# Kernel optimization log

Measured on AMD Instinct MI355X. Metric: run time of the kernel, lower is better.

## Reference

```python
import jax, jax.numpy as jnp
import numpy as np

N_NODES = 50000
N_EDGES = 100000
IN_FEATS = 63          # nodes has 64 cols: 63 features + 1 root flag
HIDDEN = 64
NUM_REL = 8
OUT_DIM = 1


def setup_inputs() -> dict:
    key = jax.random.key(0)
    k1, k2, k3, k4, k5, k6, k7 = jax.random.split(key, 7)
    nodes = jax.random.normal(k1, (N_NODES, IN_FEATS + 1), dtype=jnp.float32)
    senders = jax.random.randint(k2, (N_EDGES,), 0, N_NODES, dtype=jnp.int32)
    receivers = jax.random.randint(k3, (N_EDGES,), 0, N_NODES, dtype=jnp.int32)
    edge_types = jax.random.randint(k4, (N_EDGES,), 0, NUM_REL, dtype=jnp.int32)
    n_node = jnp.ones((1,), dtype=jnp.int32) * N_NODES
    # lecun_normal for kernels: std = 1/sqrt(fan_in)
    kernels = jax.random.normal(k5, (NUM_REL, IN_FEATS, HIDDEN), dtype=jnp.float32) / np.sqrt(IN_FEATS)
    dense_w = jax.random.normal(k6, (HIDDEN, OUT_DIM), dtype=jnp.float32) / np.sqrt(HIDDEN)
    dense_b = jnp.zeros((OUT_DIM,), dtype=jnp.float32)
    return {"nodes": nodes, "senders": senders, "receivers": receivers,
            "edge_types": edge_types, "n_node": n_node,
            "kernels": kernels, "dense_w": dense_w, "dense_b": dense_b}


def reference(nodes, senders, receivers, edge_types, n_node, kernels, dense_w, dense_b):
    num_nodes = nodes.shape[0]
    h = nodes[:, :-1]                     # [N, IN_FEATS]
    is_root = nodes[:, -1:]               # [N, 1]

    # --- single RGCN layer (hidden_dims=[64]) ---
    sender_feats = h[senders]             # [E, IN_FEATS] gather
    edge_kernels = kernels[edge_types]    # [E, IN_FEATS, HIDDEN] relation gather
    messages = jnp.einsum('eif,ei->ef', edge_kernels, sender_feats)  # [E, HIDDEN]

    ones = jnp.ones_like(senders, dtype=jnp.float32)
    sender_deg = jax.ops.segment_sum(ones, senders, num_segments=num_nodes)
    receiver_deg = jax.ops.segment_sum(ones, receivers, num_segments=num_nodes)
    norm_s = jax.lax.rsqrt(jnp.maximum(sender_deg, 1.0))
    norm_r = jax.lax.rsqrt(jnp.maximum(receiver_deg, 1.0))

    messages = messages * norm_s[senders, None]
    agg = jax.ops.segment_sum(messages, receivers, num_segments=num_nodes)
    agg = agg * norm_r[:, None]
    h = jax.nn.relu(agg)                  # [N, HIDDEN]

    # --- root pooling (num_graphs == 1) ---
    num_graphs = n_node.shape[0]
    segment_ids = jnp.repeat(jnp.arange(num_graphs), repeats=num_nodes // num_graphs)
    graph_emb = jax.ops.segment_sum(h * is_root, segment_ids, num_segments=num_graphs)  # [1, HIDDEN]

    out = graph_emb @ dense_w + dense_b   # [1, OUT_DIM]
    return jnp.squeeze(out, axis=0)
```

## Files before the change

### kernel.cpp

```cpp
#include <hip/hip_runtime.h>

#define NN 50000
#define NE 100000
#define IN_F 63
#define HID 64
#define NREL 8
#define CHUNK 64
#define R1_BLOCKS 2048

__global__ __launch_bounds__(256) void deg_kernel(const int* __restrict__ senders,
                                                  const int* __restrict__ receivers,
                                                  float* __restrict__ sdeg,
                                                  float* __restrict__ rdeg) {
    int e = blockIdx.x * 256 + threadIdx.x;
    if (e < NE) {
        atomicAdd(&sdeg[senders[e]], 1.0f);
        atomicAdd(&rdeg[receivers[e]], 1.0f);
    }
}

__global__ __launch_bounds__(256) void edge_kernel(const float* __restrict__ nodes,
                                                   const int* __restrict__ senders,
                                                   const int* __restrict__ receivers,
                                                   const int* __restrict__ etypes,
                                                   const float* __restrict__ kernels,
                                                   const float* __restrict__ sdeg,
                                                   float* __restrict__ agg) {
    const int lane = threadIdx.x & 63;
    const int t = blockIdx.x & (NREL - 1);
    const int chunk = (blockIdx.x >> 3) * 4 + (threadIdx.x >> 6);
    const int base = chunk * CHUNK;
    if (base >= NE) return;
    const int lim = min(base + CHUNK, NE);

    float kcol[IN_F];
    const float* Kt = kernels + (size_t)t * IN_F * HID;
#pragma unroll
    for (int i = 0; i < IN_F; ++i) kcol[i] = Kt[i * HID + lane];

    const int e = base + lane;
    int pack_l = 0, ty = -1, s_tmp = 0;
    if (e < lim) {
        ty     = etypes[e];
        s_tmp  = senders[e];
        pack_l = s_tmp | (receivers[e] << 16);
    }
    float ns_l = 1.0f;
    if (ty == t) ns_l = rsqrtf(fmaxf(sdeg[s_tmp], 1.0f));

    unsigned long long m = __ballot(ty == t);
    while (m) {
        const int i0 = __builtin_ctzll(m); m &= m - 1;
        const bool has2 = (m != 0);
        const int i1 = has2 ? __builtin_ctzll(m) : i0;
        if (has2) m &= m - 1;

        const int   p0  = __builtin_amdgcn_readfirstlane(__shfl(pack_l, i0));
        const float ns0 = __shfl(ns_l, i0);
        const int   p1  = __builtin_amdgcn_readfirstlane(__shfl(pack_l, i1));
        const float ns1 = __shfl(ns_l, i1);
        const int s0 = p0 & 0xFFFF, r0 = ((unsigned)p0) >> 16;
        const int s1 = p1 & 0xFFFF, r1 = ((unsigned)p1) >> 16;

        const float4* xa = (const float4*)(nodes + (size_t)s0 * (IN_F + 1));
        const float4* xb = (const float4*)(nodes + (size_t)s1 * (IN_F + 1));
        float a0 = 0.f, a1 = 0.f, a2 = 0.f, a3 = 0.f;
        float b0 = 0.f, b1 = 0.f, b2 = 0.f, b3 = 0.f;
#pragma unroll
        for (int j = 0; j < 16; ++j) {
            const float4 va = xa[j];
            const float4 vb = xb[j];
            a0 = fmaf(kcol[4 * j + 0], va.x, a0);
            a1 = fmaf(kcol[4 * j + 1], va.y, a1);
            a2 = fmaf(kcol[4 * j + 2], va.z, a2);
            if (4 * j + 3 < IN_F) a3 = fmaf(kcol[4 * j + 3], va.w, a3);
            b0 = fmaf(kcol[4 * j + 0], vb.x, b0);
            b1 = fmaf(kcol[4 * j + 1], vb.y, b1);
            b2 = fmaf(kcol[4 * j + 2], vb.z, b2);
            if (4 * j + 3 < IN_F) b3 = fmaf(kcol[4 * j + 3], vb.w, b3);
        }
        atomicAdd(&agg[(size_t)r0 * HID + lane], ((a0 + a1) + (a2 + a3)) * ns0);
        if (has2)
            atomicAdd(&agg[(size_t)r1 * HID + lane], ((b0 + b1) + (b2 + b3)) * ns1);
    }
}

__global__ __launch_bounds__(256) void readout1_kernel(const float* __restrict__ nodes,
                                                       const float* __restrict__ agg,
                                                       const float* __restrict__ rdeg,
                                                       const float* __restrict__ w,
                                                       float* __restrict__ partial) {
    __shared__ float wsum[4];
    const int lane = threadIdx.x & 63;
    const int wid  = threadIdx.x >> 6;
    const int gw = blockIdx.x * 4 + wid;
    const int nw = R1_BLOCKS * 4;
    const float wf = w[lane];

    float local = 0.f;
    for (int n = gw; n < NN; n += nw) {
        float a = agg[(size_t)n * HID + lane];
        float nr = rsqrtf(fmaxf(rdeg[n], 1.0f));
        float root = nodes[(size_t)n * (IN_F + 1) + IN_F];
        local += fmaxf(a * nr, 0.f) * root;
    }
    float v = local * wf;
#pragma unroll
    for (int o = 32; o > 0; o >>= 1) v += __shfl_xor(v, o, 64);
    if (lane == 0) wsum[wid] = v;
    __syncthreads();
    if (threadIdx.x == 0)
        partial[blockIdx.x] = (wsum[0] + wsum[1]) + (wsum[2] + wsum[3]);
}

__global__ __launch_bounds__(256) void readout2_kernel(const float* __restrict__ partial,
                                                       const float* __restrict__ b,
                                                       float* __restrict__ out) {
    __shared__ float wsum[4];
    const int lane = threadIdx.x & 63;
    const int wid  = threadIdx.x >> 6;
    float v = 0.f;
    for (int i = threadIdx.x; i < R1_BLOCKS; i += 256) v += partial[i];
#pragma unroll
    for (int o = 32; o > 0; o >>= 1) v += __shfl_xor(v, o, 64);
    if (lane == 0) wsum[wid] = v;
    __syncthreads();
    if (threadIdx.x == 0)
        out[0] = (wsum[0] + wsum[1]) + (wsum[2] + wsum[3]) + b[0];
}

extern "C" void kernel_launch(void* const* d_in, const int* in_sizes, int n_in,
                              void* d_out, int out_size, void* d_ws, size_t ws_size,
                              hipStream_t stream) {
    const float* nodes     = (const float*)d_in[0];
    const int*   senders   = (const int*)d_in[1];
    const int*   receivers = (const int*)d_in[2];
    const int*   etypes    = (const int*)d_in[3];
    const float* kernels   = (const float*)d_in[5];
    const float* dense_w   = (const float*)d_in[6];
    const float* dense_b   = (const float*)d_in[7];
    float* out = (float*)d_out;

    float* agg     = (float*)d_ws;
    float* sdeg    = agg + (size_t)NN * HID;
    float* rdeg    = sdeg + NN;
    float* partial = rdeg + NN;

    size_t zero_bytes = ((size_t)NN * HID + 2 * (size_t)NN) * sizeof(float);
    (void)hipMemsetAsync(d_ws, 0, zero_bytes, stream);

    deg_kernel<<<(NE + 255) / 256, 256, 0, stream>>>(senders, receivers, sdeg, rdeg);

    const int nchunks = (NE + CHUNK - 1) / CHUNK;
    const int cgroups = (nchunks + 3) / 4;
    const int blocks  = cgroups * NREL;
    edge_kernel<<<blocks, 256, 0, stream>>>(nodes, senders, receivers, etypes,
                                            kernels, sdeg, agg);

    readout1_kernel<<<R1_BLOCKS, 256, 0, stream>>>(nodes, agg, rdeg, dense_w, partial);
    readout2_kernel<<<1, 256, 0, stream>>>(partial, dense_b, out);
}
```

Before: 124.3 us.

## Bucket edges by relation type and compute messages per-lane with transposed kernels

Adds a counting-sort pass that groups edges by relation into padded per-type segments, with the sender norm precomputed. A transposed copy of the relation kernels lets each lane compute one edge's full 64-wide message from a register-held feature row with uniform weight loads. Messages are staged in rotated shared memory and scattered with coalesced atomics. This replaces the old scheme in which each relation block scanned every edge chunk and processed matching edges with wave-serial shuffles, at the cost of three extra small kernel launches and heavy register use per lane.

```diff
diff --git a/kernel.cpp b/kernel.cpp
--- a/kernel.cpp
+++ b/kernel.cpp
@@ -5,8 +5,9 @@
 #define IN_F 63
 #define HID 64
 #define NREL 8
-#define CHUNK 64
 #define R1_BLOCKS 2048
+#define EPAD (NE + NREL * 63)
+#define EBLKS ((EPAD + 63) / 64)
 
 __global__ __launch_bounds__(256) void deg_kernel(const int* __restrict__ senders,
                                                   const int* __restrict__ receivers,
@@ -19,69 +20,116 @@
     }
 }
 
-__global__ __launch_bounds__(256) void edge_kernel(const float* __restrict__ nodes,
-                                                   const int* __restrict__ senders,
-                                                   const int* __restrict__ receivers,
-                                                   const int* __restrict__ etypes,
-                                                   const float* __restrict__ kernels,
-                                                   const float* __restrict__ sdeg,
+__global__ __launch_bounds__(256) void ktrans_kernel(const float* __restrict__ K,
+                                                     float* __restrict__ KT) {
+    int idx = blockIdx.x * 256 + threadIdx.x;
+    if (idx < NREL * HID * IN_F) {
+        int t = idx / (HID * IN_F);
+        int rem = idx - t * (HID * IN_F);
+        int f = rem / IN_F;
+        int i = rem - f * IN_F;
+        KT[idx] = K[(size_t)t * IN_F * HID + i * HID + f];
+    }
+}
+
+__global__ __launch_bounds__(256) void rsort_kernel(const int* __restrict__ senders,
+                                                    const int* __restrict__ receivers,
+                                                    const int* __restrict__ etypes,
+                                                    const float* __restrict__ sdeg,
+                                                    int* __restrict__ gcur,
+                                                    int* __restrict__ sr32,
+                                                    float* __restrict__ ns_srt) {
+    __shared__ int lcnt[NREL], lloc[NREL];
+    if (threadIdx.x < NREL) lcnt[threadIdx.x] = 0;
+    __syncthreads();
+    const int e = blockIdx.x * 256 + threadIdx.x;
+    int t = 0, rank = 0, s = 0, r = 0;
+    if (e < NE) {
+        t = etypes[e]; s = senders[e]; r = receivers[e];
+        rank = atomicAdd(&lcnt[t], 1);
+    }
+    __syncthreads();
+    if (threadIdx.x < NREL)
+        lloc[threadIdx.x] = atomicAdd(&gcur[threadIdx.x], lcnt[threadIdx.x]);
+    __syncthreads();
+    if (e < NE) {
+        const int pos = t * NE + lloc[t] + rank;
+        sr32[pos] = s | (r << 16);
+        ns_srt[pos] = rsqrtf(fmaxf(sdeg[s], 1.0f));
+    }
+}
+
+__global__ __launch_bounds__(64) void padclear_kernel(const int* __restrict__ gcur,
+                                                      int* __restrict__ sr32,
+                                                      float* __restrict__ ns_srt) {
+    const int t = blockIdx.x;
+    const int c = gcur[t];
+    const int end = (c + 63) & ~63;
+    const int i = c + threadIdx.x;
+    if (i < end) {
+        sr32[t * NE + i] = 0;
+        ns_srt[t * NE + i] = 0.f;
+    }
+}
+
+__global__ __launch_bounds__(64) void edgeT_kernel(const float* __restrict__ nodes,
+                                                   const float* __restrict__ KT,
+                                                   const int* __restrict__ sr32,
+                                                   const float* __restrict__ ns_srt,
+                                                   const int* __restrict__ gcur,
                                                    float* __restrict__ agg) {
-    const int lane = threadIdx.x & 63;
-    const int t = blockIdx.x & (NREL - 1);
-    const int chunk = (blockIdx.x >> 3) * 4 + (threadIdx.x >> 6);
-    const int base = chunk * CHUNK;
-    if (base >= NE) return;
-    const int lim = min(base + CHUNK, NE);
-
-    float kcol[IN_F];
-    const float* Kt = kernels + (size_t)t * IN_F * HID;
-#pragma unroll
-    for (int i = 0; i < IN_F; ++i) kcol[i] = Kt[i * HID + lane];
-
-    const int e = base + lane;
-    int pack_l = 0, ty = -1, s_tmp = 0;
-    if (e < lim) {
-        ty     = etypes[e];
-        s_tmp  = senders[e];
-        pack_l = s_tmp | (receivers[e] << 16);
-    }
-    float ns_l = 1.0f;
-    if (ty == t) ns_l = rsqrtf(fmaxf(sdeg[s_tmp], 1.0f));
-
-    unsigned long long m = __ballot(ty == t);
-    while (m) {
-        const int i0 = __builtin_ctzll(m); m &= m - 1;
-        const bool has2 = (m != 0);
-        const int i1 = has2 ? __builtin_ctzll(m) : i0;
-        if (has2) m &= m - 1;
-
-        const int   p0  = __builtin_amdgcn_readfirstlane(__shfl(pack_l, i0));
-        const float ns0 = __shfl(ns_l, i0);
-        const int   p1  = __builtin_amdgcn_readfirstlane(__shfl(pack_l, i1));
-        const float ns1 = __shfl(ns_l, i1);
-        const int s0 = p0 & 0xFFFF, r0 = ((unsigned)p0) >> 16;
-        const int s1 = p1 & 0xFFFF, r1 = ((unsigned)p1) >> 16;
-
-        const float4* xa = (const float4*)(nodes + (size_t)s0 * (IN_F + 1));
-        const float4* xb = (const float4*)(nodes + (size_t)s1 * (IN_F + 1));
+    __shared__ float outb[64 * HID];
+    const int lane = threadIdx.x;
+
+    int base = 0, t = -1, local = 0;
+#pragma unroll
+    for (int tt = 0; tt < NREL; ++tt) {
+        const int seg = (gcur[tt] + 63) & ~63;
+        if (t < 0 && blockIdx.x * 64 < base + seg) { t = tt; local = blockIdx.x * 64 - base; }
+        base += seg;
+    }
+    if (t < 0) return;
+
+    const int e = t * NE + local + lane;
+    const int sr = sr32[e];
+    const float nsv = ns_srt[e];
+    const int s = sr & 0xFFFF;
+
+    float x[HID];
+    const float4* x4 = (const float4*)(nodes + (size_t)s * HID);
+#pragma unroll
+    for (int j = 0; j < 16; ++j) {
+        const float4 v = x4[j];
+        x[4 * j + 0] = v.x; x[4 * j + 1] = v.y;
+        x[4 * j + 2] = v.z; x[4 * j + 3] = v.w;
+    }
+
+    const float* KTt = KT + (size_t)t * HID * IN_F;
+#pragma unroll 2
+    for (int f = 0; f < HID; ++f) {
+        const float* kf = KTt + f * IN_F;
         float a0 = 0.f, a1 = 0.f, a2 = 0.f, a3 = 0.f;
-        float b0 = 0.f, b1 = 0.f, b2 = 0.f, b3 = 0.f;
-#pragma unroll
-        for (int j = 0; j < 16; ++j) {
-            const float4 va = xa[j];
-            const float4 vb = xb[j];
-            a0 = fmaf(kcol[4 * j + 0], va.x, a0);
-            a1 = fmaf(kcol[4 * j + 1], va.y, a1);
-            a2 = fmaf(kcol[4 * j + 2], va.z, a2);
-            if (4 * j + 3 < IN_F) a3 = fmaf(kcol[4 * j + 3], va.w, a3);
-            b0 = fmaf(kcol[4 * j + 0], vb.x, b0);
-            b1 = fmaf(kcol[4 * j + 1], vb.y, b1);
-            b2 = fmaf(kcol[4 * j + 2], vb.z, b2);
-            if (4 * j + 3 < IN_F) b3 = fmaf(kcol[4 * j + 3], vb.w, b3);
+#pragma unroll
+        for (int i = 0; i < 60; i += 4) {
+            a0 = fmaf(kf[i + 0], x[i + 0], a0);
+            a1 = fmaf(kf[i + 1], x[i + 1], a1);
+            a2 = fmaf(kf[i + 2], x[i + 2], a2);
+            a3 = fmaf(kf[i + 3], x[i + 3], a3);
         }
-        atomicAdd(&agg[(size_t)r0 * HID + lane], ((a0 + a1) + (a2 + a3)) * ns0);
-        if (has2)
-            atomicAdd(&agg[(size_t)r1 * HID + lane], ((b0 + b1) + (b2 + b3)) * ns1);
+        a0 = fmaf(kf[60], x[60], a0);
+        a1 = fmaf(kf[61], x[61], a1);
+        a2 = fmaf(kf[62], x[62], a2);
+        outb[lane * HID + ((f + lane) & 63)] = (a0 + a1) + (a2 + a3);
+    }
+    __syncthreads();
+
+    const int r_l = ((unsigned)sr) >> 16;
+    for (int e2 = 0; e2 < 64; ++e2) {
+        const float nsu = __shfl(nsv, e2);
+        if (nsu == 0.f) continue;
+        const int rr = __shfl(r_l, e2);
+        const float val = outb[e2 * HID + ((lane + e2) & 63)];
+        atomicAdd(&agg[(size_t)rr * HID + lane], val * nsu);
     }
 }
 
@@ -101,7 +149,7 @@
     for (int n = gw; n < NN; n += nw) {
         float a = agg[(size_t)n * HID + lane];
         float nr = rsqrtf(fmaxf(rdeg[n], 1.0f));
-        float root = nodes[(size_t)n * (IN_F + 1) + IN_F];
+        float root = nodes[(size_t)n * HID + IN_F];
         local += fmaxf(a * nr, 0.f) * root;
     }
     float v = local * wf;
@@ -145,17 +193,21 @@
     float* sdeg    = agg + (size_t)NN * HID;
     float* rdeg    = sdeg + NN;
     float* partial = rdeg + NN;
-
-    size_t zero_bytes = ((size_t)NN * HID + 2 * (size_t)NN) * sizeof(float);
+    int*   gcur    = (int*)(partial + R1_BLOCKS);
+    int*   sr32    = gcur + NREL;
+    float* ns_srt  = (float*)(sr32 + (size_t)NREL * NE);
+    float* KT      = ns_srt + (size_t)NREL * NE;
+
+    size_t zero_bytes = ((size_t)NN * HID + 2 * NN + R1_BLOCKS) * sizeof(float)
+                      + NREL * sizeof(int);
     (void)hipMemsetAsync(d_ws, 0, zero_bytes, stream);
 
     deg_kernel<<<(NE + 255) / 256, 256, 0, stream>>>(senders, receivers, sdeg, rdeg);
-
-    const int nchunks = (NE + CHUNK - 1) / CHUNK;
-    const int cgroups = (nchunks + 3) / 4;
-    const int blocks  = cgroups * NREL;
-    edge_kernel<<<blocks, 256, 0, stream>>>(nodes, senders, receivers, etypes,
-                                            kernels, sdeg, agg);
+    ktrans_kernel<<<(NREL * HID * IN_F + 255) / 256, 256, 0, stream>>>(kernels, KT);
+    rsort_kernel<<<(NE + 255) / 256, 256, 0, stream>>>(senders, receivers, etypes,
+                                                       sdeg, gcur, sr32, ns_srt);
+    padclear_kernel<<<NREL, 64, 0, stream>>>(gcur, sr32, ns_srt);
+    edgeT_kernel<<<EBLKS, 64, 0, stream>>>(nodes, KT, sr32, ns_srt, gcur, agg);
 
     readout1_kernel<<<R1_BLOCKS, 256, 0, stream>>>(nodes, agg, rdeg, dense_w, partial);
     readout2_kernel<<<1, 256, 0, stream>>>(partial, dense_b, out);
```

Measured after the change: 197.6 us. +58.9%, slower.
